# Performance work log

Hardware: AMD Instinct MI355X
Metric: run time of the kernel (lower is better)

## Reference

```python
import jax, jax.numpy as jnp
import numpy as np


def setup_inputs() -> dict:
    key = jax.random.key(0)
    k1, k2, k3 = jax.random.split(key, 3)
    shape = (32, 3, 512, 512)
    inp = jax.random.normal(k1, shape, dtype=jnp.float32)
    tgt = jax.random.normal(k2, shape, dtype=jnp.float32)
    mask = jax.random.randint(k3, shape, 0, 2, dtype=jnp.int32)
    return {"input": inp, "target": tgt, "mask": mask}


def reference(input, target, mask):
    # masked MSE: mean of squared diff over elements where mask == 1
    diff2 = (input - target) ** 2
    m = (mask == 1).astype(diff2.dtype)
    sum2 = jnp.sum(diff2 * m)
    num = jnp.sum(m)
    return sum2 / num
```

## Files before the change

### kernel.cpp

```cpp
#include <hip/hip_runtime.h>


#define BLOCK 256
#define GRID 2048

__global__ __launch_bounds__(BLOCK) void masked_mse_reduce(
    const float4* __restrict__ inp,
    const float4* __restrict__ tgt,
    const int4* __restrict__ msk,
    float* __restrict__ acc_sum,
    unsigned int* __restrict__ acc_cnt,
    int n4)
{
    int idx = blockIdx.x * blockDim.x + threadIdx.x;
    int stride = gridDim.x * blockDim.x;

    float s = 0.0f;
    unsigned int c = 0u;

    for (int i = idx; i < n4; i += stride) {
        float4 a = inp[i];
        float4 b = tgt[i];
        int4 m = msk[i];
        float d0 = a.x - b.x;
        float d1 = a.y - b.y;
        float d2 = a.z - b.z;
        float d3 = a.w - b.w;
        s += (float)m.x * d0 * d0;
        s += (float)m.y * d1 * d1;
        s += (float)m.z * d2 * d2;
        s += (float)m.w * d3 * d3;
        c += (unsigned int)(m.x + m.y + m.z + m.w);
    }

    #pragma unroll
    for (int off = 32; off > 0; off >>= 1) {
        s += __shfl_down(s, off, 64);
        c += __shfl_down(c, off, 64);
    }

    __shared__ float ssum[BLOCK / 64];
    __shared__ unsigned int scnt[BLOCK / 64];
    int lane = threadIdx.x & 63;
    int wave = threadIdx.x >> 6;
    if (lane == 0) {
        ssum[wave] = s;
        scnt[wave] = c;
    }
    __syncthreads();
    if (threadIdx.x == 0) {
        float bs = 0.0f;
        unsigned int bc = 0u;
        #pragma unroll
        for (int w = 0; w < BLOCK / 64; ++w) {
            bs += ssum[w];
            bc += scnt[w];
        }
        atomicAdd(acc_sum, bs);
        atomicAdd(acc_cnt, bc);
    }
}

__global__ void masked_mse_finalize(const float* __restrict__ acc_sum,
                                    const unsigned int* __restrict__ acc_cnt,
                                    float* __restrict__ out)
{
    out[0] = acc_sum[0] / (float)acc_cnt[0];
}

extern "C" void kernel_launch(void* const* d_in, const int* in_sizes, int n_in,
                              void* d_out, int out_size, void* d_ws, size_t ws_size,
                              hipStream_t stream)
{
    const float4* inp = (const float4*)d_in[0];
    const float4* tgt = (const float4*)d_in[1];
    const int4* msk = (const int4*)d_in[2];
    int n = in_sizes[0];
    int n4 = n / 4;

    float* acc_sum = (float*)d_ws;
    unsigned int* acc_cnt = (unsigned int*)((char*)d_ws + sizeof(float));

    hipMemsetAsync(d_ws, 0, sizeof(float) + sizeof(unsigned int), stream);

    masked_mse_reduce<<<GRID, BLOCK, 0, stream>>>(inp, tgt, msk, acc_sum, acc_cnt, n4);
    masked_mse_finalize<<<1, 1, 0, stream>>>(acc_sum, acc_cnt, (float*)d_out);
}
```

Before: 286.3 us.

## Replace grid-stride loop with one-shot unrolled blocks plus tail kernel

Drops the fixed 2048-block grid-stride loop. Each block now handles a fixed chunk of BLOCK*8 float4 elements, with all loads issued up front to raise memory-level parallelism. A separate tail kernel covers any remainder. The grid becomes large (about 3000 blocks for this size), so atomic traffic on the single accumulator rises and more blocks must be launched.

```diff
diff --git a/kernel.cpp b/kernel.cpp
--- a/kernel.cpp
+++ b/kernel.cpp
@@ -2,38 +2,44 @@
 
 
 #define BLOCK 256
-#define GRID 2048
+#define UNROLL 8
 
 __global__ __launch_bounds__(BLOCK) void masked_mse_reduce(
     const float4* __restrict__ inp,
     const float4* __restrict__ tgt,
     const int4* __restrict__ msk,
     float* __restrict__ acc_sum,
-    unsigned int* __restrict__ acc_cnt,
-    int n4)
+    unsigned int* __restrict__ acc_cnt)
 {
-    int idx = blockIdx.x * blockDim.x + threadIdx.x;
-    int stride = gridDim.x * blockDim.x;
+    const long base = (long)blockIdx.x * (BLOCK * UNROLL) + threadIdx.x;
+
+    float4 a[UNROLL];
+    float4 b[UNROLL];
+    int4 m[UNROLL];
+#pragma unroll
+    for (int u = 0; u < UNROLL; ++u) {
+        const long i = base + (long)u * BLOCK;
+        a[u] = inp[i];
+        b[u] = tgt[i];
+        m[u] = msk[i];
+    }
 
     float s = 0.0f;
     unsigned int c = 0u;
-
-    for (int i = idx; i < n4; i += stride) {
-        float4 a = inp[i];
-        float4 b = tgt[i];
-        int4 m = msk[i];
-        float d0 = a.x - b.x;
-        float d1 = a.y - b.y;
-        float d2 = a.z - b.z;
-        float d3 = a.w - b.w;
-        s += (float)m.x * d0 * d0;
-        s += (float)m.y * d1 * d1;
-        s += (float)m.z * d2 * d2;
-        s += (float)m.w * d3 * d3;
-        c += (unsigned int)(m.x + m.y + m.z + m.w);
+#pragma unroll
+    for (int u = 0; u < UNROLL; ++u) {
+        float d0 = a[u].x - b[u].x;
+        float d1 = a[u].y - b[u].y;
+        float d2 = a[u].z - b[u].z;
+        float d3 = a[u].w - b[u].w;
+        s += (float)m[u].x * d0 * d0;
+        s += (float)m[u].y * d1 * d1;
+        s += (float)m[u].z * d2 * d2;
+        s += (float)m[u].w * d3 * d3;
+        c += (unsigned int)(m[u].x + m[u].y + m[u].z + m[u].w);
     }
 
-    #pragma unroll
+#pragma unroll
     for (int off = 32; off > 0; off >>= 1) {
         s += __shfl_down(s, off, 64);
         c += __shfl_down(c, off, 64);
@@ -41,8 +47,8 @@
 
     __shared__ float ssum[BLOCK / 64];
     __shared__ unsigned int scnt[BLOCK / 64];
-    int lane = threadIdx.x & 63;
-    int wave = threadIdx.x >> 6;
+    const int lane = threadIdx.x & 63;
+    const int wave = threadIdx.x >> 6;
     if (lane == 0) {
         ssum[wave] = s;
         scnt[wave] = c;
@@ -51,13 +57,41 @@
     if (threadIdx.x == 0) {
         float bs = 0.0f;
         unsigned int bc = 0u;
-        #pragma unroll
+#pragma unroll
         for (int w = 0; w < BLOCK / 64; ++w) {
             bs += ssum[w];
             bc += scnt[w];
         }
         atomicAdd(acc_sum, bs);
         atomicAdd(acc_cnt, bc);
+    }
+}
+
+__global__ void masked_mse_tail(
+    const float* __restrict__ inp,
+    const float* __restrict__ tgt,
+    const int* __restrict__ msk,
+    float* __restrict__ acc_sum,
+    unsigned int* __restrict__ acc_cnt,
+    long start, long n)
+{
+    long i = start + blockIdx.x * (long)blockDim.x + threadIdx.x;
+    float s = 0.0f;
+    unsigned int c = 0u;
+    for (; i < n; i += (long)gridDim.x * blockDim.x) {
+        float d = inp[i] - tgt[i];
+        int mv = msk[i];
+        s += (float)mv * d * d;
+        c += (unsigned int)mv;
+    }
+#pragma unroll
+    for (int off = 32; off > 0; off >>= 1) {
+        s += __shfl_down(s, off, 64);
+        c += __shfl_down(c, off, 64);
+    }
+    if ((threadIdx.x & 63) == 0) {
+        atomicAdd(acc_sum, s);
+        atomicAdd(acc_cnt, c);
     }
 }
 
@@ -72,17 +106,28 @@
                               void* d_out, int out_size, void* d_ws, size_t ws_size,
                               hipStream_t stream)
 {
-    const float4* inp = (const float4*)d_in[0];
-    const float4* tgt = (const float4*)d_in[1];
-    const int4* msk = (const int4*)d_in[2];
-    int n = in_sizes[0];
-    int n4 = n / 4;
+    const float* inp = (const float*)d_in[0];
+    const float* tgt = (const float*)d_in[1];
+    const int* msk = (const int*)d_in[2];
+    const long n = in_sizes[0];
+    const long n4 = n / 4;
 
     float* acc_sum = (float*)d_ws;
     unsigned int* acc_cnt = (unsigned int*)((char*)d_ws + sizeof(float));
 
-    hipMemsetAsync(d_ws, 0, sizeof(float) + sizeof(unsigned int), stream);
+    hipMemsetAsync(d_ws, 0, 2 * sizeof(float), stream);
 
-    masked_mse_reduce<<<GRID, BLOCK, 0, stream>>>(inp, tgt, msk, acc_sum, acc_cnt, n4);
+    const long per_block = (long)BLOCK * UNROLL;
+    const long nblocks = n4 / per_block;
+    if (nblocks > 0) {
+        masked_mse_reduce<<<(int)nblocks, BLOCK, 0, stream>>>(
+            (const float4*)inp, (const float4*)tgt, (const int4*)msk,
+            acc_sum, acc_cnt);
+    }
+    const long covered = nblocks * per_block * 4;
+    if (covered < n) {
+        masked_mse_tail<<<64, BLOCK, 0, stream>>>(
+            inp, tgt, msk, acc_sum, acc_cnt, covered, n);
+    }
     masked_mse_finalize<<<1, 1, 0, stream>>>(acc_sum, acc_cnt, (float*)d_out);
 }
```

Result: no change. 284.1 us (-0.8%).
